# Kernel optimization log

Measured on AMD Instinct MI355X. Metric: run time of the kernel, lower is better.

## Reference

```python
import jax, jax.numpy as jnp
import numpy as np

MARGIN = 0.5
B, D, P = 4096, 4096, 8


def setup_inputs() -> dict:
    key = jax.random.key(0)
    kx, kp = jax.random.split(key)
    x = jax.random.normal(kx, (B, D), dtype=jnp.float32)
    pos_ids = jax.random.randint(kp, (B, P), 0, D, dtype=jnp.int64)
    # y is the multi-hot label vector consistent with pos_ids: y[i, k] = 1 for k in pos_ids[i]
    y = jnp.zeros((B, D), dtype=jnp.float32)
    y = y.at[jnp.arange(B)[:, None], pos_ids].set(1.0)
    return {"x": x, "y": y, "pos_ids": pos_ids}


def reference(x, y, pos_ids):
    # x: [B, D] scores, y: [B, D] multi-hot labels, pos_ids: [B, P] positive indices
    x_pos = jnp.take_along_axis(x, pos_ids, axis=1)              # [B, P] anchor scores x[i, k]
    # margin violations: relu(margin + x[i, d] - x[i, k]) for every (k, d) pair
    viol = jnp.maximum(0.0, MARGIN + x[:, None, :] - x_pos[:, :, None])  # [B, P, D]
    # (1 - y[i]) masks out positive classes from the negative side
    loss = jnp.sum((1.0 - y)[:, None, :] * viol)
    count = B * P * (D - P)  # original: sum_i sum_{k in pos_ids[i]} (D - len(pos_ids[i]))
    return loss / count
```

## Files before the change

kernel.cpp:

```cpp
#include <hip/hip_runtime.h>
#include <hip/hip_bf16.h>

#define MB 4096
#define MD 4096
#define MP 8
#define MARGIN 0.5f

typedef float f32x4 __attribute__((ext_vector_type(4)));

__global__ __launch_bounds__(256) void margin_rows_kernel(
    const float* __restrict__ x,
    const int* __restrict__ pos_ids,
    float* __restrict__ ws)
{
    const int row = blockIdx.x;
    const int t = threadIdx.x;
    const int lane = t & 63;
    const float* __restrict__ xr = x + (size_t)row * MD;

    const int p = pos_ids[row * MP + (lane & 7)];

    const f32x4* __restrict__ xr4 = reinterpret_cast<const f32x4*>(xr);
    const f32x4 v0 = __builtin_nontemporal_load(xr4 + t);
    const f32x4 v1 = __builtin_nontemporal_load(xr4 + 256 + t);
    const f32x4 v2 = __builtin_nontemporal_load(xr4 + 512 + t);
    const f32x4 v3 = __builtin_nontemporal_load(xr4 + 768 + t);

    const float xg = xr[p];

    float th[MP];
    int   pi[MP];
#pragma unroll
    for (int k = 0; k < MP; ++k) {
        th[k] = __shfl(xg, k, 64) - MARGIN;
        pi[k] = __shfl(p, k, 64);
    }

    const float vv[16] = { v0.x, v0.y, v0.z, v0.w,
                           v1.x, v1.y, v1.z, v1.w,
                           v2.x, v2.y, v2.z, v2.w,
                           v3.x, v3.y, v3.z, v3.w };

    float acc0 = 0.0f, acc1 = 0.0f;
#pragma unroll
    for (int j = 0; j < 16; ++j) {
        const float v = vv[j];
#pragma unroll
        for (int k = 0; k < MP; k += 2) {
            acc0 += fmaxf(0.0f, v - th[k]);
            acc1 += fmaxf(0.0f, v - th[k + 1]);
        }
    }
    float acc = acc0 + acc1;

#pragma unroll
    for (int off = 32; off > 0; off >>= 1)
        acc += __shfl_down(acc, off, 64);

    __shared__ float s_part[4];
    const int wave = t >> 6;
    if ((t & 63) == 0) s_part[wave] = acc;
    __syncthreads();

    if (t == 0) {
        const float total = s_part[0] + s_part[1] + s_part[2] + s_part[3];
        float corr = 0.0f;
#pragma unroll
        for (int k = 0; k < MP; ++k) {
            bool dup = false;
#pragma unroll
            for (int k2 = 0; k2 < k; ++k2) dup = dup || (pi[k2] == pi[k]);
            if (!dup) {
                const float xk = th[k] + MARGIN;
#pragma unroll
                for (int j = 0; j < MP; ++j)
                    corr += fmaxf(0.0f, xk - th[j]);
            }
        }
        ws[row] = total - corr;
    }
}

__global__ __launch_bounds__(256) void margin_final_kernel(
    const float* __restrict__ ws,
    float* __restrict__ out)
{
    const int t = threadIdx.x;
    double acc = 0.0;
#pragma unroll
    for (int it = 0; it < 16; ++it)
        acc += (double)ws[it * 256 + t];

#pragma unroll
    for (int off = 32; off > 0; off >>= 1)
        acc += __shfl_down(acc, off, 64);

    __shared__ double s_part[4];
    const int wave = t >> 6;
    if ((t & 63) == 0) s_part[wave] = acc;
    __syncthreads();
    if (t == 0) {
        const double tot = s_part[0] + s_part[1] + s_part[2] + s_part[3];
        const double count = (double)MB * (double)MP * (double)(MD - MP);
        out[0] = (float)(tot / count);
    }
}

extern "C" void kernel_launch(void* const* d_in, const int* in_sizes, int n_in,
                              void* d_out, int out_size, void* d_ws, size_t ws_size,
                              hipStream_t stream) {
    const float* x = (const float*)d_in[0];
    const int* pos_ids = (const int*)d_in[2];
    float* out = (float*)d_out;
    float* ws = (float*)d_ws;

    margin_rows_kernel<<<MB, 256, 0, stream>>>(x, pos_ids, ws);
    margin_final_kernel<<<1, 256, 0, stream>>>(ws, out);
}
```

Measured before the change: 19.74 us.

## Fuse final reduction via last-block atomic ticket and process four rows per block

Merges the per-row and final reduction kernels into one kernel where each block handles four rows, publishes a block partial, and the last block to take an atomic ticket performs the double-precision final sum. The duplicate-positive correction is spread over the first eight threads instead of a serial loop on thread 0. This removes a second kernel launch and reduces block count, at the cost of a memset launch for the counter and an atomic serialization point.

```diff
diff --git a/kernel.cpp b/kernel.cpp
--- a/kernel.cpp
+++ b/kernel.cpp
@@ -5,104 +5,114 @@
 #define MD 4096
 #define MP 8
 #define MARGIN 0.5f
+#define ROWS 4
+#define NB (MB / ROWS)
 
 typedef float f32x4 __attribute__((ext_vector_type(4)));
 
-__global__ __launch_bounds__(256) void margin_rows_kernel(
+__global__ __launch_bounds__(256) void margin_fused_kernel(
     const float* __restrict__ x,
     const int* __restrict__ pos_ids,
-    float* __restrict__ ws)
+    float* __restrict__ partials,
+    int* __restrict__ counter,
+    float* __restrict__ out)
 {
-    const int row = blockIdx.x;
     const int t = threadIdx.x;
     const int lane = t & 63;
-    const float* __restrict__ xr = x + (size_t)row * MD;
+    const int wave = t >> 6;
+    const int row0 = blockIdx.x * ROWS;
 
-    const int p = pos_ids[row * MP + (lane & 7)];
+    float acc0 = 0.0f, acc1 = 0.0f;
 
-    const f32x4* __restrict__ xr4 = reinterpret_cast<const f32x4*>(xr);
-    const f32x4 v0 = __builtin_nontemporal_load(xr4 + t);
-    const f32x4 v1 = __builtin_nontemporal_load(xr4 + 256 + t);
-    const f32x4 v2 = __builtin_nontemporal_load(xr4 + 512 + t);
-    const f32x4 v3 = __builtin_nontemporal_load(xr4 + 768 + t);
+#pragma unroll
+    for (int r = 0; r < ROWS; ++r) {
+        const int row = row0 + r;
+        const float* __restrict__ xr = x + (size_t)row * MD;
 
-    const float xg = xr[p];
+        const int p = pos_ids[row * MP + (lane & 7)];
 
-    float th[MP];
-    int   pi[MP];
+        const f32x4* __restrict__ xr4 = reinterpret_cast<const f32x4*>(xr);
+        const f32x4 v0 = __builtin_nontemporal_load(xr4 + t);
+        const f32x4 v1 = __builtin_nontemporal_load(xr4 + 256 + t);
+        const f32x4 v2 = __builtin_nontemporal_load(xr4 + 512 + t);
+        const f32x4 v3 = __builtin_nontemporal_load(xr4 + 768 + t);
+
+        const float xg = xr[p];
+
+        float th[MP];
+        int   pi[MP];
 #pragma unroll
-    for (int k = 0; k < MP; ++k) {
-        th[k] = __shfl(xg, k, 64) - MARGIN;
-        pi[k] = __shfl(p, k, 64);
+        for (int k = 0; k < MP; ++k) {
+            th[k] = __shfl(xg, k, 64) - MARGIN;
+            pi[k] = __shfl(p, k, 64);
+        }
+
+        const float vv[16] = { v0.x, v0.y, v0.z, v0.w,
+                               v1.x, v1.y, v1.z, v1.w,
+                               v2.x, v2.y, v2.z, v2.w,
+                               v3.x, v3.y, v3.z, v3.w };
+
+#pragma unroll
+        for (int j = 0; j < 16; ++j) {
+            const float v = vv[j];
+#pragma unroll
+            for (int k = 0; k < MP; k += 2) {
+                acc0 += fmaxf(0.0f, v - th[k]);
+                acc1 += fmaxf(0.0f, v - th[k + 1]);
+            }
+        }
+
+        if (t < MP) {
+            bool dup = false;
+#pragma unroll
+            for (int k2 = 0; k2 < MP; ++k2) dup = dup || (k2 < t && pi[k2] == pi[t]);
+            if (!dup) {
+                const float xk = th[t] + MARGIN;
+#pragma unroll
+                for (int j = 0; j < MP; ++j)
+                    acc0 -= fmaxf(0.0f, xk - th[j]);
+            }
+        }
     }
 
-    const float vv[16] = { v0.x, v0.y, v0.z, v0.w,
-                           v1.x, v1.y, v1.z, v1.w,
-                           v2.x, v2.y, v2.z, v2.w,
-                           v3.x, v3.y, v3.z, v3.w };
-
-    float acc0 = 0.0f, acc1 = 0.0f;
-#pragma unroll
-    for (int j = 0; j < 16; ++j) {
-        const float v = vv[j];
-#pragma unroll
-        for (int k = 0; k < MP; k += 2) {
-            acc0 += fmaxf(0.0f, v - th[k]);
-            acc1 += fmaxf(0.0f, v - th[k + 1]);
-        }
-    }
     float acc = acc0 + acc1;
-
 #pragma unroll
     for (int off = 32; off > 0; off >>= 1)
         acc += __shfl_down(acc, off, 64);
 
     __shared__ float s_part[4];
-    const int wave = t >> 6;
+    __shared__ int s_last;
     if ((t & 63) == 0) s_part[wave] = acc;
     __syncthreads();
 
     if (t == 0) {
-        const float total = s_part[0] + s_part[1] + s_part[2] + s_part[3];
-        float corr = 0.0f;
+        const float bp = s_part[0] + s_part[1] + s_part[2] + s_part[3];
+        __hip_atomic_store(&partials[blockIdx.x], bp,
+                           __ATOMIC_RELAXED, __HIP_MEMORY_SCOPE_AGENT);
+        const int ticket = __hip_atomic_fetch_add(counter, 1,
+                           __ATOMIC_ACQ_REL, __HIP_MEMORY_SCOPE_AGENT);
+        s_last = (ticket == NB - 1);
+    }
+    __syncthreads();
+
+    if (s_last) {
+        double d = 0.0;
 #pragma unroll
-        for (int k = 0; k < MP; ++k) {
-            bool dup = false;
+        for (int it = 0; it < NB / 256; ++it)
+            d += (double)__hip_atomic_load(&partials[it * 256 + t],
+                         __ATOMIC_RELAXED, __HIP_MEMORY_SCOPE_AGENT);
 #pragma unroll
-            for (int k2 = 0; k2 < k; ++k2) dup = dup || (pi[k2] == pi[k]);
-            if (!dup) {
-                const float xk = th[k] + MARGIN;
-#pragma unroll
-                for (int j = 0; j < MP; ++j)
-                    corr += fmaxf(0.0f, xk - th[j]);
-            }
+        for (int off = 32; off > 0; off >>= 1)
+            d += __shfl_down(d, off, 64);
+
+        __shared__ double s_d[4];
+        if ((t & 63) == 0) s_d[wave] = d;
+        __syncthreads();
+        if (t == 0) {
+            const double tot = s_d[0] + s_d[1] + s_d[2] + s_d[3];
+            const double count = (double)MB * (double)MP * (double)(MD - MP);
+            out[0] = (float)(tot / count);
         }
-        ws[row] = total - corr;
-    }
-}
-
-__global__ __launch_bounds__(256) void margin_final_kernel(
-    const float* __restrict__ ws,
-    float* __restrict__ out)
-{
-    const int t = threadIdx.x;
-    double acc = 0.0;
-#pragma unroll
-    for (int it = 0; it < 16; ++it)
-        acc += (double)ws[it * 256 + t];
-
-#pragma unroll
-    for (int off = 32; off > 0; off >>= 1)
-        acc += __shfl_down(acc, off, 64);
-
-    __shared__ double s_part[4];
-    const int wave = t >> 6;
-    if ((t & 63) == 0) s_part[wave] = acc;
-    __syncthreads();
-    if (t == 0) {
-        const double tot = s_part[0] + s_part[1] + s_part[2] + s_part[3];
-        const double count = (double)MB * (double)MP * (double)(MD - MP);
-        out[0] = (float)(tot / count);
     }
 }
 
@@ -112,8 +122,10 @@
     const float* x = (const float*)d_in[0];
     const int* pos_ids = (const int*)d_in[2];
     float* out = (float*)d_out;
-    float* ws = (float*)d_ws;
 
-    margin_rows_kernel<<<MB, 256, 0, stream>>>(x, pos_ids, ws);
-    margin_final_kernel<<<1, 256, 0, stream>>>(ws, out);
+    int* counter = (int*)d_ws;
+    float* partials = (float*)((char*)d_ws + 256);
+
+    hipMemsetAsync(counter, 0, sizeof(int), stream);
+    margin_fused_kernel<<<NB, 256, 0, stream>>>(x, pos_ids, partials, counter, out);
 }
```

Result: slower. 53.18 us (+169.3%).
